# Performance work log

Measured on AMD Instinct MI355X. Metric: run time of the kernel, lower is better.

## Reference

```python
import jax, jax.numpy as jnp
import numpy as np

B, T, C, H = 8, 1024, 1024, 16  # batch, seq, n_embd, n_head


def setup_inputs() -> dict:
    key = jax.random.key(0)
    ks = jax.random.split(key, 5)
    scale = 1.0 / np.sqrt(C)
    return {
        "x": jax.random.normal(ks[0], (B, T, C), dtype=jnp.float32),
        "Wqkv": jax.random.normal(ks[1], (C, 3 * C), dtype=jnp.float32) * scale,
        "bqkv": jax.random.normal(ks[2], (3 * C,), dtype=jnp.float32) * 0.02,
        "Wproj": jax.random.normal(ks[3], (C, C), dtype=jnp.float32) * scale,
        "bproj": jax.random.normal(ks[4], (C,), dtype=jnp.float32) * 0.02,
        "n_head": H,
    }


def reference(x, Wqkv, bqkv, Wproj, bproj, n_head):
    Bb, Tt, Cc = x.shape
    hd = Cc // n_head  # head dim
    qkv = x @ Wqkv + bqkv                      # [B,T,3C]
    q, k, v = jnp.split(qkv, 3, axis=-1)       # each [B,T,C]
    # [B,T,C] -> [B,H,T,hd]
    def to_heads(t):
        return t.reshape(Bb, Tt, n_head, hd).transpose(0, 2, 1, 3)
    q, k, v = to_heads(q), to_heads(k), to_heads(v)
    scores = jnp.einsum("bhqd,bhkd->bhqk", q, k) / jnp.sqrt(jnp.asarray(hd, q.dtype))
    causal = jnp.tril(jnp.ones((Tt, Tt), dtype=bool))
    scores = jnp.where(causal, scores, jnp.asarray(-jnp.inf, scores.dtype))
    attn = jax.nn.softmax(scores, axis=-1)
    y = jnp.einsum("bhqk,bhkd->bhqd", attn, v)  # [B,H,T,hd]
    y = y.transpose(0, 2, 1, 3).reshape(Bb, Tt, Cc)
    return y @ Wproj + bproj
```

## Files before the change

### kernel.cpp

```cpp
#include <hip/hip_runtime.h>
#include <hip/hip_bf16.h>
#include <math.h>
#include <type_traits>

#define Bz 8
#define Tz 1024
#define Cz 1024
#define Hz 16
#define HDz 64
#define Mz (Bz*Tz)
#define N1 (3*Cz)
#define QKN 2048

typedef __attribute__((ext_vector_type(8))) short short8;
typedef __attribute__((ext_vector_type(4))) short short4v;
typedef __attribute__((ext_vector_type(4))) float floatx4;

__device__ __forceinline__ unsigned short f2bf(float f) {
    unsigned u = __float_as_uint(f);
    return (unsigned short)((u + 0x7FFFu + ((u >> 16) & 1u)) >> 16);
}

__device__ __forceinline__ unsigned pkbf(float a, float b) {
    __hip_bfloat162 h = __float22bfloat162_rn(make_float2(a, b));
    return *(unsigned*)&h;
}

__device__ __forceinline__ void gload16(const void* g, void* l) {
    __builtin_amdgcn_global_load_lds(
        (const __attribute__((address_space(1))) unsigned int*)g,
        (__attribute__((address_space(3))) unsigned int*)l, 16, 0, 0);
}

__global__ __launch_bounds__(256) void prep_kernel(
    const float* __restrict__ x, unsigned short* __restrict__ xb,
    const float* __restrict__ Wqkv, unsigned short* __restrict__ Wqkvt,
    const float* __restrict__ Wproj, unsigned short* __restrict__ Wprojt)
{
    __shared__ float tile[32][33];
    const int bid = blockIdx.x;
    const int tid = threadIdx.x;
    if (bid < 8192) {
        int i = bid * 256 + tid;
        float4 v = *(const float4*)&x[(size_t)i * 4];
        ushort4 o;
        o.x = f2bf(v.x); o.y = f2bf(v.y); o.z = f2bf(v.z); o.w = f2bf(v.w);
        *(ushort4*)&xb[(size_t)i * 4] = o;
        return;
    }
    const float* W; unsigned short* Wt; int K, N, n0, k0;
    if (bid < 11264) {
        int b = bid - 8192;  W = Wqkv;  Wt = Wqkvt;  K = Cz; N = N1;
        n0 = (b % 96) * 32;  k0 = (b / 96) * 32;
    } else {
        int b = bid - 11264; W = Wproj; Wt = Wprojt; K = Cz; N = Cz;
        n0 = (b % 32) * 32;  k0 = (b / 32) * 32;
    }
    const int tx = tid & 31, ty = tid >> 5;
#pragma unroll
    for (int i = 0; i < 4; ++i)
        tile[ty + i * 8][tx] = W[(size_t)(k0 + ty + i * 8) * N + n0 + tx];
    __syncthreads();
#pragma unroll
    for (int i = 0; i < 4; ++i)
        Wt[(size_t)(n0 + ty + i * 8) * K + k0 + tx] = f2bf(tile[tx][ty + i * 8]);
}

__global__ __launch_bounds__(256) void gemm_kernel(const unsigned short* __restrict__ A,
    const unsigned short* __restrict__ Bt, const float* __restrict__ bias,
    void* __restrict__ Cout, unsigned short* __restrict__ VtG,
    int M, int N, int K, int mode)
{
    __shared__ unsigned short As[128 * 64];
    __shared__ unsigned short Bs[128 * 64];
    const int tid = threadIdx.x;
    const int lane = tid & 63;
    const int w = tid >> 6, wr = w >> 1, wc = w & 1;
    const int quad = lane >> 4, m16 = lane & 15;
    const int row0 = blockIdx.y * 128, col0 = blockIdx.x * 128;

    float bv[4];
#pragma unroll
    for (int ni = 0; ni < 4; ++ni)
        bv[ni] = bias[col0 + wc * 64 + ni * 16 + m16];

    floatx4 acc[4][4];
#pragma unroll
    for (int mi = 0; mi < 4; ++mi)
#pragma unroll
        for (int ni = 0; ni < 4; ++ni)
            acc[mi][ni] = (floatx4){0.f, 0.f, 0.f, 0.f};

    const int l3 = lane >> 3;
    const int swz = ((lane & 7) ^ l3) * 8;
    const unsigned short* gA[4];
    const unsigned short* gB[4];
    unsigned short* lA[4];
    unsigned short* lB[4];
#pragma unroll
    for (int i = 0; i < 4; ++i) {
        int c = w * 4 + i;
        gA[i] = A  + (size_t)(row0 + c * 8 + l3) * K + swz;
        gB[i] = Bt + (size_t)(col0 + c * 8 + l3) * K + swz;
        lA[i] = &As[c * 512];
        lB[i] = &Bs[c * 512];
    }
    const int sw7 = m16 & 7;

    for (int k0 = 0; k0 < K; k0 += 64) {
#pragma unroll
        for (int i = 0; i < 4; ++i) {
            gload16(gA[i] + k0, lA[i]);
            gload16(gB[i] + k0, lB[i]);
        }
        __syncthreads();
#pragma unroll
        for (int s = 0; s < 2; ++s) {
            short8 af[4], bfr[4];
            const int ch = ((s * 4 + quad) ^ sw7) * 8;
#pragma unroll
            for (int mi = 0; mi < 4; ++mi)
                af[mi] = *(short8*)&As[(wr * 64 + mi * 16 + m16) * 64 + ch];
#pragma unroll
            for (int ni = 0; ni < 4; ++ni)
                bfr[ni] = *(short8*)&Bs[(wc * 64 + ni * 16 + m16) * 64 + ch];
#pragma unroll
            for (int mi = 0; mi < 4; ++mi)
#pragma unroll
                for (int ni = 0; ni < 4; ++ni)
                    acc[mi][ni] = __builtin_amdgcn_mfma_f32_16x16x32_bf16(af[mi], bfr[ni], acc[mi][ni], 0, 0, 0);
        }
        __syncthreads();
    }

    if (mode == 0) {
#pragma unroll
        for (int mi = 0; mi < 4; ++mi)
#pragma unroll
            for (int ni = 0; ni < 4; ++ni)
#pragma unroll
                for (int reg = 0; reg < 4; ++reg) {
                    int r = row0 + wr * 64 + mi * 16 + quad * 4 + reg;
                    int c = col0 + wc * 64 + ni * 16 + m16;
                    ((float*)Cout)[(size_t)r * N + c] = acc[mi][ni][reg] + bv[ni];
                }
    } else if (col0 < 2048) {
#pragma unroll
        for (int mi = 0; mi < 4; ++mi)
#pragma unroll
            for (int ni = 0; ni < 4; ++ni)
#pragma unroll
                for (int reg = 0; reg < 4; ++reg) {
                    int r = row0 + wr * 64 + mi * 16 + quad * 4 + reg;
                    int c = col0 + wc * 64 + ni * 16 + m16;
                    ((unsigned short*)Cout)[(size_t)r * QKN + c] = f2bf(acc[mi][ni][reg] + bv[ni]);
                }
    } else {
        const int hb = (col0 - 2048) >> 6;
        const int bq = row0 >> 10;
        const int hsel = hb + wc;
        const int d = (hsel & 15) * 0;
        (void)d;
#pragma unroll
        for (int ni = 0; ni < 4; ++ni) {
            const int dd = ni * 16 + m16;
            unsigned short* drow = VtG
                + (size_t)(bq * Hz + hsel) * (HDz * Tz)
                + (size_t)dd * Tz + (row0 & 1023);
#pragma unroll
            for (int mi = 0; mi < 4; ++mi) {
                const int t = wr * 64 + mi * 16 + quad * 4;
                unsigned pk[2];
                pk[0] = pkbf(acc[mi][ni][0] + bv[ni], acc[mi][ni][1] + bv[ni]);
                pk[1] = pkbf(acc[mi][ni][2] + bv[ni], acc[mi][ni][3] + bv[ni]);
                *(uint2*)&drow[t] = *(uint2*)pk;
            }
        }
    }
}

__global__ __launch_bounds__(128) void attn_kernel(const unsigned short* __restrict__ qkb,
    const unsigned short* __restrict__ VtG, unsigned short* __restrict__ attb)
{
    __shared__ unsigned short Ks[2][64 * 64];
    __shared__ unsigned short Vs[2][64 * 64];

    const int bx = blockIdx.x;
    const int bh = blockIdx.y;
    const int b = bh >> 4, h = bh & 15;
    const int tid = threadIdx.x, lane = tid & 63, w = tid >> 6;
    const int quad = lane >> 4, m16 = lane & 15;
    const int qis[2] = {15 - bx, bx};

    const unsigned short* Kb = qkb + (size_t)(b * Tz) * QKN + Cz + h * HDz;
    const unsigned short* Vb = VtG + (size_t)bh * (HDz * Tz);

    const int l3 = lane >> 3, l7 = lane & 7;
    const int gsw = ((l7 ^ l3) << 3);
    const int sw = m16 & 7;
    const int p0 = (quad ^ sw) << 3;

    short8 onesf = (short8){0,0,0,0,0,0,0,0};
    if (m16 == 0) {
        const short one = (short)0x3F80;
        onesf = (short8){one,one,one,one,one,one,one,one};
    }

    int srow[4];
#pragma unroll
    for (int i = 0; i < 4; ++i) srow[i] = w * 32 + i * 8 + l3;

#pragma unroll
    for (int i = 0; i < 4; ++i) {
        gload16(Kb + (size_t)srow[i] * QKN + gsw, &Ks[0][(w * 4 + i) * 512]);
        gload16(Vb + (size_t)srow[i] * Tz + gsw, &Vs[0][(w * 4 + i) * 512]);
    }

    int buf = 0;
    for (int t = 0; t < 2; ++t) {
        const int qi = qis[t];

        short8 qf[2][2];
        int qrow[2];
#pragma unroll
        for (int mi = 0; mi < 2; ++mi) {
            qrow[mi] = qi * 64 + w * 32 + mi * 16 + m16;
            const size_t rq = (size_t)(b * Tz + qrow[mi]) * QKN + h * HDz;
            qf[mi][0] = *(const short8*)&qkb[rq + quad * 8];
            qf[mi][1] = *(const short8*)&qkb[rq + 32 + quad * 8];
        }

        floatx4 of[2][4];
#pragma unroll
        for (int mi = 0; mi < 2; ++mi)
#pragma unroll
            for (int dc = 0; dc < 4; ++dc) of[mi][dc] = (floatx4){0.f, 0.f, 0.f, 0.f};
        floatx4 lsum[2];
        lsum[0] = (floatx4){0.f, 0.f, 0.f, 0.f};
        lsum[1] = (floatx4){0.f, 0.f, 0.f, 0.f};

        auto tile_body = [&](auto diag_c) {
            constexpr bool DIAG = decltype(diag_c)::value;
            short8 pf[2][2];
#pragma unroll
            for (int m0 = 0; m0 < 4; ++m0) {
                if (DIAG && w == 0 && m0 >= 2) continue;
                const unsigned short* kr = &Ks[buf][(m0 * 16 + m16) * 64];
                short8 kf0 = *(const short8*)&kr[p0];
                short8 kf1 = *(const short8*)&kr[p0 ^ 32];
#pragma unroll
                for (int mi = 0; mi < 2; ++mi) {
                    floatx4 st = (floatx4){0.f, 0.f, 0.f, 0.f};
                    st = __builtin_amdgcn_mfma_f32_16x16x32_bf16(kf0, qf[mi][0], st, 0, 0, 0);
                    st = __builtin_amdgcn_mfma_f32_16x16x32_bf16(kf1, qf[mi][1], st, 0, 0, 0);
                    float p[4];
#pragma unroll
                    for (int reg = 0; reg < 4; ++reg) {
                        p[reg] = exp2f(st[reg] * 0.18033688f);
                        if (DIAG) {
                            int key = m0 * 16 + quad * 4 + reg;
                            int qr  = w * 32 + mi * 16 + m16;
                            p[reg] = (key <= qr) ? p[reg] : 0.f;
                        }
                    }
                    unsigned* pp = (unsigned*)&pf[mi][m0 >> 1];
                    pp[(m0 & 1) * 2 + 0] = pkbf(p[0], p[1]);
                    pp[(m0 & 1) * 2 + 1] = pkbf(p[2], p[3]);
                }
            }
#pragma unroll
            for (int kg = 0; kg < 2; ++kg) {
                if (DIAG && w == 0 && kg == 1) continue;
#pragma unroll
                for (int mi = 0; mi < 2; ++mi)
                    lsum[mi] = __builtin_amdgcn_mfma_f32_16x16x32_bf16(onesf, pf[mi][kg], lsum[mi], 0, 0, 0);
#pragma unroll
                for (int dc = 0; dc < 4; ++dc) {
                    const unsigned short* vrow = &Vs[buf][(dc * 16 + m16) * 64];
                    const int g0 = kg * 4 + (quad >> 1);
                    const int off = (quad & 1) * 4;
                    short4v v0 = *(const short4v*)&vrow[((g0 ^ sw) << 3) + off];
                    short4v v1 = *(const short4v*)&vrow[(((g0 + 2) ^ sw) << 3) + off];
                    short8 vf;
                    vf[0] = v0[0]; vf[1] = v0[1]; vf[2] = v0[2]; vf[3] = v0[3];
                    vf[4] = v1[0]; vf[5] = v1[1]; vf[6] = v1[2]; vf[7] = v1[3];
#pragma unroll
                    for (int mi = 0; mi < 2; ++mi)
                        of[mi][dc] = __builtin_amdgcn_mfma_f32_16x16x32_bf16(vf, pf[mi][kg], of[mi][dc], 0, 0, 0);
                }
            }
        };

        for (int ki = 0; ki <= qi; ++ki) {
            __syncthreads();
            const int nk = (ki < qi) ? (ki + 1) : (t == 0 ? 0 : -1);
            if (nk >= 0) {
                const size_t ko = (size_t)nk * 64;
#pragma unroll
                for (int i = 0; i < 4; ++i) {
                    gload16(Kb + (ko + srow[i]) * QKN + gsw, &Ks[buf ^ 1][(w * 4 + i) * 512]);
                    gload16(Vb + (size_t)srow[i] * Tz + ko + gsw, &Vs[buf ^ 1][(w * 4 + i) * 512]);
                }
            }
            if (ki == qi) tile_body(std::true_type{});
            else          tile_body(std::false_type{});
            buf ^= 1;
        }

#pragma unroll
        for (int mi = 0; mi < 2; ++mi) {
            const float l = __shfl(lsum[mi][0], m16);
            const float inv = 1.f / l;
            const size_t orow = (size_t)(b * Tz + qrow[mi]) * Cz + h * HDz;
#pragma unroll
            for (int dc = 0; dc < 4; ++dc) {
                ushort4 o;
                o.x = f2bf(of[mi][dc][0] * inv);
                o.y = f2bf(of[mi][dc][1] * inv);
                o.z = f2bf(of[mi][dc][2] * inv);
                o.w = f2bf(of[mi][dc][3] * inv);
                *(ushort4*)&attb[orow + dc * 16 + quad * 4] = o;
            }
        }
    }
}

extern "C" void kernel_launch(void* const* d_in, const int* in_sizes, int n_in,
                              void* d_out, int out_size, void* d_ws, size_t ws_size,
                              hipStream_t stream)
{
    const float* x     = (const float*)d_in[0];
    const float* Wqkv  = (const float*)d_in[1];
    const float* bqkv  = (const float*)d_in[2];
    const float* Wproj = (const float*)d_in[3];
    const float* bproj = (const float*)d_in[4];
    float* out = (float*)d_out;

    unsigned short* xb     = (unsigned short*)d_ws;
    unsigned short* Wqkvt  = xb + (size_t)Mz * Cz;
    unsigned short* Wprojt = Wqkvt + (size_t)N1 * Cz;
    unsigned short* qkb    = Wprojt + (size_t)Cz * Cz;
    unsigned short* VtG    = qkb + (size_t)Mz * QKN;
    unsigned short* attb   = xb;

    prep_kernel<<<12288, 256, 0, stream>>>(x, xb, Wqkv, Wqkvt, Wproj, Wprojt);

    gemm_kernel<<<dim3(N1 / 128, Mz / 128), 256, 0, stream>>>(
        xb, Wqkvt, bqkv, qkb, VtG, Mz, N1, Cz, 2);

    attn_kernel<<<dim3(8, Bz * Hz), 128, 0, stream>>>(qkb, VtG, attb);

    gemm_kernel<<<dim3(Cz / 128, Mz / 128), 256, 0, stream>>>(
        attb, Wprojt, bproj, out, nullptr, Mz, Cz, Cz, 0);
}
```

Measured before the change: 246.9 us.

## Replace QKV GEMM with 256x256-tile, 8-wave, double-buffered pipelined kernel

The QKV projection now runs in a new kernel with 256x256 output tiles, 512 threads and a double-buffered LDS pipeline. Global loads for later k-steps are interleaved with MFMA phases, and barriers, waitcnt and setprio are placed by hand. A workgroup index remap groups tiles for cache locality. The goal is more data reuse per tile and global loads hidden behind compute, at the cost of heavy register pressure (128 accumulators per thread), large LDS use and low occupancy.

Result: no change. 249.9 us (+1.2%).

```diff
diff --git a/kernel.cpp b/kernel.cpp
--- a/kernel.cpp
+++ b/kernel.cpp
@@ -144,32 +144,149 @@
                     int c = col0 + wc * 64 + ni * 16 + m16;
                     ((float*)Cout)[(size_t)r * N + c] = acc[mi][ni][reg] + bv[ni];
                 }
-    } else if (col0 < 2048) {
-#pragma unroll
-        for (int mi = 0; mi < 4; ++mi)
-#pragma unroll
-            for (int ni = 0; ni < 4; ++ni)
+    }
+}
+
+__global__ __launch_bounds__(512) void gemm256_qkv(const unsigned short* __restrict__ A,
+    const unsigned short* __restrict__ Bt, const float* __restrict__ bias,
+    unsigned short* __restrict__ Cqk, unsigned short* __restrict__ VtG)
+{
+    __shared__ unsigned short lds[2 * 2 * 2 * 8192];
+    constexpr int NT = 16;
+
+    const int tid = threadIdx.x;
+    const int lane = tid & 63;
+    const int w = tid >> 6;
+    const int wm = w >> 2, wn = w & 3;
+    const int quad = lane >> 4, m16 = lane & 15;
+    const int sw7 = m16 & 7;
+
+    int wg = blockIdx.x;
+    wg = (wg & 7) * 48 + (wg >> 3);
+    const int bx = wg % 12, by = wg / 12;
+    const int row0 = by * 256, col0 = bx * 256;
+
+    const int srow = tid >> 3;
+    const int scol = ((tid & 7) ^ (srow & 7)) * 8;
+    const unsigned short* sA[2][2];
+    const unsigned short* sB[2][2];
+#pragma unroll
+    for (int h = 0; h < 2; ++h)
+#pragma unroll
+        for (int c = 0; c < 2; ++c) {
+            sA[h][c] = A  + (size_t)(row0 + h * 128 + c * 64 + srow) * Cz + scol;
+            sB[h][c] = Bt + (size_t)(col0 + h * 128 + c * 64 + srow) * Cz + scol;
+        }
+
+    auto stage = [&](int mat, int h, int kt, int db) {
+        const unsigned short* s0 = (mat ? sB[h][0] : sA[h][0]) + kt * 64;
+        const unsigned short* s1 = (mat ? sB[h][1] : sA[h][1]) + kt * 64;
+        unsigned short* d = &lds[db * 32768 + mat * 16384 + h * 8192 + w * 512];
+        gload16(s0, d);
+        gload16(s1, d + 4096);
+    };
+
+    float bv[4];
+#pragma unroll
+    for (int ni = 0; ni < 4; ++ni)
+        bv[ni] = bias[col0 + wn * 64 + ni * 16 + m16];
+
+    floatx4 acc[8][4];
+#pragma unroll
+    for (int mi = 0; mi < 8; ++mi)
+#pragma unroll
+        for (int ni = 0; ni < 4; ++ni)
+            acc[mi][ni] = (floatx4){0.f, 0.f, 0.f, 0.f};
+
+    stage(1, 0, 0, 0); stage(1, 1, 0, 0); stage(0, 0, 0, 0); stage(0, 1, 0, 0);
+    stage(1, 0, 1, 1); stage(1, 1, 1, 1); stage(0, 0, 1, 1);
+    asm volatile("s_waitcnt vmcnt(6)" ::: "memory");
+    __builtin_amdgcn_s_barrier();
+
+    const int rB0 = ((wn & 1) * 64 + m16) * 64;
+    const int lBoff = 16384 + (wn >> 1) * 8192;
+
+    auto tile_step = [&](const int b, const int kt) {
+        const unsigned short* lA = &lds[b * 32768];
+        const unsigned short* lB = &lds[b * 32768 + lBoff];
+        short8 bfr[4][2];
+#pragma unroll
+        for (int p = 0; p < 4; ++p) {
+            const int hf = p >> 1;
+            short8 af[2][2];
+#pragma unroll
+            for (int j = 0; j < 2; ++j) {
+                const int ra = ((p & 1) * 64 + j * 32 + wm * 16 + m16) * 64;
+#pragma unroll
+                for (int ks = 0; ks < 2; ++ks)
+                    af[j][ks] = *(const short8*)&lA[hf * 8192 + ra + ((((ks << 2) | quad) ^ sw7) << 3)];
+            }
+            if (p == 0) {
+#pragma unroll
+                for (int ni = 0; ni < 4; ++ni)
+#pragma unroll
+                    for (int ks = 0; ks < 2; ++ks)
+                        bfr[ni][ks] = *(const short8*)&lB[rB0 + ni * 1024 + ((((ks << 2) | quad) ^ sw7) << 3)];
+                if (kt + 1 < NT) stage(0, 1, kt + 1, b ^ 1);
+            } else if (kt + 2 < NT) {
+                if (p == 1)      stage(1, 0, kt + 2, b);
+                else if (p == 2) stage(1, 1, kt + 2, b);
+                else             stage(0, 0, kt + 2, b);
+            }
+            __builtin_amdgcn_s_barrier();
+            asm volatile("s_waitcnt lgkmcnt(0)" ::: "memory");
+            __builtin_amdgcn_sched_barrier(0);
+            __builtin_amdgcn_s_setprio(1);
+#pragma unroll
+            for (int ks = 0; ks < 2; ++ks)
+#pragma unroll
+                for (int j = 0; j < 2; ++j)
+#pragma unroll
+                    for (int ni = 0; ni < 4; ++ni)
+                        acc[p * 2 + j][ni] = __builtin_amdgcn_mfma_f32_16x16x32_bf16(
+                            af[j][ks], bfr[ni][ks], acc[p * 2 + j][ni], 0, 0, 0);
+            __builtin_amdgcn_s_setprio(0);
+            if (p == 3) {
+                if (kt < NT - 2) { asm volatile("s_waitcnt vmcnt(6)" ::: "memory"); }
+                else             { asm volatile("s_waitcnt vmcnt(0)" ::: "memory"); }
+            }
+            __builtin_amdgcn_s_barrier();
+        }
+    };
+
+#pragma unroll 1
+    for (int j = 0; j < 7; ++j) {
+        tile_step(0, 2 * j);
+        tile_step(1, 2 * j + 1);
+    }
+    tile_step(0, 14);
+    tile_step(1, 15);
+
+    if (bx < 8) {
+#pragma unroll
+        for (int mi = 0; mi < 8; ++mi)
+#pragma unroll
+            for (int ni = 0; ni < 4; ++ni) {
+                const int c = col0 + wn * 64 + ni * 16 + m16;
 #pragma unroll
                 for (int reg = 0; reg < 4; ++reg) {
-                    int r = row0 + wr * 64 + mi * 16 + quad * 4 + reg;
-                    int c = col0 + wc * 64 + ni * 16 + m16;
-                    ((unsigned short*)Cout)[(size_t)r * QKN + c] = f2bf(acc[mi][ni][reg] + bv[ni]);
+                    const int r = row0 + mi * 32 + wm * 16 + quad * 4 + reg;
+                    Cqk[(size_t)r * QKN + c] = f2bf(acc[mi][ni][reg] + bv[ni]);
                 }
+            }
     } else {
-        const int hb = (col0 - 2048) >> 6;
+        const int hsel = (bx - 8) * 4 + wn;
         const int bq = row0 >> 10;
-        const int hsel = hb + wc;
-        const int d = (hsel & 15) * 0;
-        (void)d;
+        const int tb = row0 & 1023;
 #pragma unroll
         for (int ni = 0; ni < 4; ++ni) {
             const int dd = ni * 16 + m16;
             unsigned short* drow = VtG
                 + (size_t)(bq * Hz + hsel) * (HDz * Tz)
-                + (size_t)dd * Tz + (row0 & 1023);
-#pragma unroll
-            for (int mi = 0; mi < 4; ++mi) {
-                const int t = wr * 64 + mi * 16 + quad * 4;
+                + (size_t)dd * Tz + tb;
+#pragma unroll
+            for (int mi = 0; mi < 8; ++mi) {
+                const int t = mi * 32 + wm * 16 + quad * 4;
                 unsigned pk[2];
                 pk[0] = pkbf(acc[mi][ni][0] + bv[ni], acc[mi][ni][1] + bv[ni]);
                 pk[1] = pkbf(acc[mi][ni][2] + bv[ni], acc[mi][ni][3] + bv[ni]);
@@ -345,8 +462,8 @@
 
     prep_kernel<<<12288, 256, 0, stream>>>(x, xb, Wqkv, Wqkvt, Wproj, Wprojt);
 
-    gemm_kernel<<<dim3(N1 / 128, Mz / 128), 256, 0, stream>>>(
-        xb, Wqkvt, bqkv, qkb, VtG, Mz, N1, Cz, 2);
+    gemm256_qkv<<<(N1 / 256) * (Mz / 256), 512, 0, stream>>>(
+        xb, Wqkvt, bqkv, qkb, VtG);
 
     attn_kernel<<<dim3(8, Bz * Hz), 128, 0, stream>>>(qkb, VtG, attb);
 
```

## Rewrite GEMMs as 8-wave double-buffered kernels with XCD-aware block mapping

Applied to the files above, without the earlier changes.

Replaces the 128x128 single-buffered GEMM with a templated 512-thread kernel that computes 256xNI*64 tiles (256x192 for the QKV projection, 256x128 for the output projection). It double-buffers LDS with global_load_lds prefetch two tiles ahead, uses manual vmcnt/lgkmcnt waits and sched barriers to interleave LDS fragment loads with MFMA clusters, and raises wave priority during the MFMA clusters. Block IDs are remapped across the 8 XCDs for L2 locality. This is meant to hide global and LDS latency and raise MFMA utilisation, but the launch drops to 512 and 256 blocks. The larger LDS footprint and register count also reduce occupancy.

Measured after the change: 236.0 us. 1.05x faster.

```diff
diff --git a/kernel.cpp b/kernel.cpp
--- a/kernel.cpp
+++ b/kernel.cpp
@@ -15,6 +15,8 @@
 typedef __attribute__((ext_vector_type(8))) short short8;
 typedef __attribute__((ext_vector_type(4))) short short4v;
 typedef __attribute__((ext_vector_type(4))) float floatx4;
+
+template<int V> using IC = std::integral_constant<int, V>;
 
 __device__ __forceinline__ unsigned short f2bf(float f) {
     unsigned u = __float_as_uint(f);
@@ -66,114 +68,190 @@
         Wt[(size_t)(n0 + ty + i * 8) * K + k0 + tx] = f2bf(tile[tx][ty + i * 8]);
 }
 
-__global__ __launch_bounds__(256) void gemm_kernel(const unsigned short* __restrict__ A,
-    const unsigned short* __restrict__ Bt, const float* __restrict__ bias,
-    void* __restrict__ Cout, unsigned short* __restrict__ VtG,
-    int M, int N, int K, int mode)
+template<int NI, int MODE, int NXB>
+__global__ __launch_bounds__(512) void gemm8p(
+    const unsigned short* __restrict__ A,
+    const unsigned short* __restrict__ Bt,
+    const float* __restrict__ bias,
+    void* __restrict__ Cout, unsigned short* __restrict__ VtG)
 {
-    __shared__ unsigned short As[128 * 64];
-    __shared__ unsigned short Bs[128 * 64];
+    constexpr int LDSB = 16384 + NI * 4096;
+    constexpr int NT = 16;
+    constexpr int NBLK = (Mz / 256) * NXB;
+    constexpr int CHUNK = NBLK / 8;
+    constexpr int NOUT = NXB * NI * 64;
+    __shared__ unsigned short lds[2 * LDSB];
+
     const int tid = threadIdx.x;
     const int lane = tid & 63;
-    const int w = tid >> 6, wr = w >> 1, wc = w & 1;
+    const int w = tid >> 6;
+    const int wm = w >> 2, wn = w & 3;
     const int quad = lane >> 4, m16 = lane & 15;
-    const int row0 = blockIdx.y * 128, col0 = blockIdx.x * 128;
-
-    float bv[4];
-#pragma unroll
-    for (int ni = 0; ni < 4; ++ni)
-        bv[ni] = bias[col0 + wc * 64 + ni * 16 + m16];
-
-    floatx4 acc[4][4];
-#pragma unroll
-    for (int mi = 0; mi < 4; ++mi)
-#pragma unroll
-        for (int ni = 0; ni < 4; ++ni)
+    const int sw7 = m16 & 7;
+
+    int wg = blockIdx.x;
+    wg = (wg & 7) * CHUNK + (wg >> 3);
+    const int bx = wg % NXB, by = wg / NXB;
+    const int row0 = by * 256, col0 = bx * (NI * 64);
+
+    const int srow = tid >> 3;
+    const int scol = ((tid & 7) ^ (srow & 7)) * 8;
+    const unsigned short* sA[2][2];
+    const unsigned short* sBu[NI];
+#pragma unroll
+    for (int h = 0; h < 2; ++h)
+#pragma unroll
+        for (int c = 0; c < 2; ++c)
+            sA[h][c] = A + (size_t)(row0 + h * 128 + c * 64 + srow) * Cz + scol;
+#pragma unroll
+    for (int u = 0; u < NI; ++u)
+        sBu[u] = Bt + (size_t)(col0 + u * 64 + srow) * Cz + scol;
+
+    auto stage_tile = [&](int kt, int db) {
+        unsigned short* base = &lds[db * LDSB];
+#pragma unroll
+        for (int u = 0; u < NI; ++u)
+            gload16(sBu[u] + kt * 64, base + 16384 + u * 4096 + w * 512);
+        gload16(sA[0][0] + kt * 64, base + w * 512);
+        gload16(sA[0][1] + kt * 64, base + w * 512 + 4096);
+        gload16(sA[1][0] + kt * 64, base + 8192 + w * 512);
+        gload16(sA[1][1] + kt * 64, base + 8192 + w * 512 + 4096);
+    };
+
+    float bv[NI];
+#pragma unroll
+    for (int ni = 0; ni < NI; ++ni)
+        bv[ni] = bias[col0 + wn * (NI * 16) + ni * 16 + m16];
+
+    floatx4 acc[8][NI];
+#pragma unroll
+    for (int mi = 0; mi < 8; ++mi)
+#pragma unroll
+        for (int ni = 0; ni < NI; ++ni)
             acc[mi][ni] = (floatx4){0.f, 0.f, 0.f, 0.f};
 
-    const int l3 = lane >> 3;
-    const int swz = ((lane & 7) ^ l3) * 8;
-    const unsigned short* gA[4];
-    const unsigned short* gB[4];
-    unsigned short* lA[4];
-    unsigned short* lB[4];
-#pragma unroll
-    for (int i = 0; i < 4; ++i) {
-        int c = w * 4 + i;
-        gA[i] = A  + (size_t)(row0 + c * 8 + l3) * K + swz;
-        gB[i] = Bt + (size_t)(col0 + c * 8 + l3) * K + swz;
-        lA[i] = &As[c * 512];
-        lB[i] = &Bs[c * 512];
-    }
-    const int sw7 = m16 & 7;
-
-    for (int k0 = 0; k0 < K; k0 += 64) {
-#pragma unroll
-        for (int i = 0; i < 4; ++i) {
-            gload16(gA[i] + k0, lA[i]);
-            gload16(gB[i] + k0, lB[i]);
-        }
-        __syncthreads();
-#pragma unroll
-        for (int s = 0; s < 2; ++s) {
-            short8 af[4], bfr[4];
-            const int ch = ((s * 4 + quad) ^ sw7) * 8;
-#pragma unroll
-            for (int mi = 0; mi < 4; ++mi)
-                af[mi] = *(short8*)&As[(wr * 64 + mi * 16 + m16) * 64 + ch];
-#pragma unroll
-            for (int ni = 0; ni < 4; ++ni)
-                bfr[ni] = *(short8*)&Bs[(wc * 64 + ni * 16 + m16) * 64 + ch];
-#pragma unroll
-            for (int mi = 0; mi < 4; ++mi)
-#pragma unroll
-                for (int ni = 0; ni < 4; ++ni)
-                    acc[mi][ni] = __builtin_amdgcn_mfma_f32_16x16x32_bf16(af[mi], bfr[ni], acc[mi][ni], 0, 0, 0);
-        }
-        __syncthreads();
-    }
-
-    if (mode == 0) {
-#pragma unroll
-        for (int mi = 0; mi < 4; ++mi)
-#pragma unroll
-            for (int ni = 0; ni < 4; ++ni)
+    stage_tile(0, 0);
+    stage_tile(1, 1);
+
+    int b = 0;
+#pragma unroll 1
+    for (int kt = 0; kt < NT; ++kt, b ^= 1) {
+        if (kt < NT - 1) {
+            if constexpr (NI == 3) asm volatile("s_waitcnt vmcnt(7)" ::: "memory");
+            else                   asm volatile("s_waitcnt vmcnt(6)" ::: "memory");
+        } else {
+            asm volatile("s_waitcnt vmcnt(0)" ::: "memory");
+        }
+        asm volatile("s_barrier" ::: "memory");
+
+        const unsigned short* lA = &lds[b * LDSB];
+        const unsigned short* lB = &lds[b * LDSB + 16384];
+
+        auto loadA = [&](auto pc, short8 (&af)[2][2]) {
+            constexpr int p = decltype(pc)::value;
+            constexpr int hf = p >> 1;
+#pragma unroll
+            for (int j = 0; j < 2; ++j) {
+                const int ra = ((p & 1) * 64 + j * 32 + wm * 16 + m16) * 64;
+#pragma unroll
+                for (int ks = 0; ks < 2; ++ks)
+                    af[j][ks] = *(const short8*)&lA[hf * 8192 + ra + ((((ks << 2) | quad) ^ sw7) << 3)];
+            }
+        };
+
+        short8 bfr[NI][2];
+#pragma unroll
+        for (int ni = 0; ni < NI; ++ni) {
+            const int rb = (wn * (NI * 16) + ni * 16 + m16) * 64;
+#pragma unroll
+            for (int ks = 0; ks < 2; ++ks)
+                bfr[ni][ks] = *(const short8*)&lB[rb + ((((ks << 2) | quad) ^ sw7) << 3)];
+        }
+
+        auto cluster = [&](auto pc, short8 (&af)[2][2]) {
+            constexpr int p = decltype(pc)::value;
+            __builtin_amdgcn_s_setprio(1);
+#pragma unroll
+            for (int ks = 0; ks < 2; ++ks)
+#pragma unroll
+                for (int j = 0; j < 2; ++j)
+#pragma unroll
+                    for (int ni = 0; ni < NI; ++ni)
+                        acc[p * 2 + j][ni] = __builtin_amdgcn_mfma_f32_16x16x32_bf16(
+                            af[j][ks], bfr[ni][ks], acc[p * 2 + j][ni], 0, 0, 0);
+            __builtin_amdgcn_s_setprio(0);
+        };
+
+        short8 afA[2][2], afB[2][2];
+        loadA(IC<0>{}, afA);
+        __builtin_amdgcn_sched_barrier(0);
+        loadA(IC<1>{}, afB);
+        __builtin_amdgcn_sched_barrier(0);
+        asm volatile("s_waitcnt lgkmcnt(4)" ::: "memory");
+        __builtin_amdgcn_sched_barrier(0);
+        cluster(IC<0>{}, afA);
+        loadA(IC<2>{}, afA);
+        __builtin_amdgcn_sched_barrier(0);
+        asm volatile("s_waitcnt lgkmcnt(4)" ::: "memory");
+        __builtin_amdgcn_sched_barrier(0);
+        cluster(IC<1>{}, afB);
+        loadA(IC<3>{}, afB);
+        __builtin_amdgcn_sched_barrier(0);
+        asm volatile("s_waitcnt lgkmcnt(4)" ::: "memory");
+        __builtin_amdgcn_sched_barrier(0);
+        cluster(IC<2>{}, afA);
+        asm volatile("s_waitcnt lgkmcnt(0)" ::: "memory");
+        __builtin_amdgcn_sched_barrier(0);
+        if (kt + 2 < NT) {
+            asm volatile("s_barrier" ::: "memory");
+            stage_tile(kt + 2, b);
+        }
+        __builtin_amdgcn_sched_barrier(0);
+        cluster(IC<3>{}, afB);
+    }
+
+    if constexpr (MODE == 0) {
+#pragma unroll
+        for (int ni = 0; ni < NI; ++ni) {
+            const int c = col0 + wn * (NI * 16) + ni * 16 + m16;
+#pragma unroll
+            for (int mi = 0; mi < 8; ++mi)
 #pragma unroll
                 for (int reg = 0; reg < 4; ++reg) {
-                    int r = row0 + wr * 64 + mi * 16 + quad * 4 + reg;
-                    int c = col0 + wc * 64 + ni * 16 + m16;
-                    ((float*)Cout)[(size_t)r * N + c] = acc[mi][ni][reg] + bv[ni];
+                    const int r = row0 + mi * 32 + wm * 16 + quad * 4 + reg;
+                    ((float*)Cout)[(size_t)r * NOUT + c] = acc[mi][ni][reg] + bv[ni];
                 }
-    } else if (col0 < 2048) {
-#pragma unroll
-        for (int mi = 0; mi < 4; ++mi)
-#pragma unroll
-            for (int ni = 0; ni < 4; ++ni)
-#pragma unroll
-                for (int reg = 0; reg < 4; ++reg) {
-                    int r = row0 + wr * 64 + mi * 16 + quad * 4 + reg;
-                    int c = col0 + wc * 64 + ni * 16 + m16;
-                    ((unsigned short*)Cout)[(size_t)r * QKN + c] = f2bf(acc[mi][ni][reg] + bv[ni]);
+        }
+    } else {
+#pragma unroll
+        for (int ni = 0; ni < NI; ++ni) {
+            const int c0 = col0 + wn * (NI * 16) + ni * 16;
+            if (c0 < 2048) {
+#pragma unroll
+                for (int mi = 0; mi < 8; ++mi)
+#pragma unroll
+                    for (int reg = 0; reg < 4; ++reg) {
+                        const int r = row0 + mi * 32 + wm * 16 + quad * 4 + reg;
+                        ((unsigned short*)Cout)[(size_t)r * QKN + c0 + m16] =
+                            f2bf(acc[mi][ni][reg] + bv[ni]);
+                    }
+            } else {
+                const int cb = c0 - 2048;
+                const int hsel = cb >> 6;
+                const int dd = (cb & 63) + m16;
+                const int bq = row0 >> 10;
+                const int tb = row0 & 1023;
+                unsigned short* drow = VtG
+                    + (size_t)(bq * Hz + hsel) * (HDz * Tz)
+                    + (size_t)dd * Tz + tb;
+#pragma unroll
+                for (int mi = 0; mi < 8; ++mi) {
+                    const int t = mi * 32 + wm * 16 + quad * 4;
+                    unsigned pk[2];
+                    pk[0] = pkbf(acc[mi][ni][0] + bv[ni], acc[mi][ni][1] + bv[ni]);
+                    pk[1] = pkbf(acc[mi][ni][2] + bv[ni], acc[mi][ni][3] + bv[ni]);
+                    *(uint2*)&drow[t] = *(uint2*)pk;
                 }
-    } else {
-        const int hb = (col0 - 2048) >> 6;
-        const int bq = row0 >> 10;
-        const int hsel = hb + wc;
-        const int d = (hsel & 15) * 0;
-        (void)d;
-#pragma unroll
-        for (int ni = 0; ni < 4; ++ni) {
-            const int dd = ni * 16 + m16;
-            unsigned short* drow = VtG
-                + (size_t)(bq * Hz + hsel) * (HDz * Tz)
-                + (size_t)dd * Tz + (row0 & 1023);
-#pragma unroll
-            for (int mi = 0; mi < 4; ++mi) {
-                const int t = wr * 64 + mi * 16 + quad * 4;
-                unsigned pk[2];
-                pk[0] = pkbf(acc[mi][ni][0] + bv[ni], acc[mi][ni][1] + bv[ni]);
-                pk[1] = pkbf(acc[mi][ni][2] + bv[ni], acc[mi][ni][3] + bv[ni]);
-                *(uint2*)&drow[t] = *(uint2*)pk;
             }
         }
     }
@@ -345,11 +423,9 @@
 
     prep_kernel<<<12288, 256, 0, stream>>>(x, xb, Wqkv, Wqkvt, Wproj, Wprojt);
 
-    gemm_kernel<<<dim3(N1 / 128, Mz / 128), 256, 0, stream>>>(
-        xb, Wqkvt, bqkv, qkb, VtG, Mz, N1, Cz, 2);
+    gemm8p<3, 2, 16><<<512, 512, 0, stream>>>(xb, Wqkvt, bqkv, qkb, VtG);
 
     attn_kernel<<<dim3(8, Bz * Hz), 128, 0, stream>>>(qkb, VtG, attb);
 
-    gemm_kernel<<<dim3(Cz / 128, Mz / 128), 256, 0, stream>>>(
-        attb, Wprojt, bproj, out, nullptr, Mz, Cz, Cz, 0);
-}
+    gemm8p<2, 0, 8><<<256, 512, 0, stream>>>(attb, Wprojt, bproj, out, nullptr);
+}
```
